# Kernel tuning notes

Measured on AMD Instinct MI355X. Metric: run time of the kernel, lower is better.

## Reference

```python
import jax, jax.numpy as jnp
import numpy as np

B, C, H, W = 1, 256, 48, 64
HW = H * W
HIDDEN, CTX = 128, 64
LEVELS, RADIUS = 4, 4
WIN = 2 * RADIUS + 1
P = WIN * WIN                     # 81 lookup points per level
CORR_DIM = P * LEVELS             # 324
TOP_K = 3
ITERS = 4
STEP_ROT, STEP_TRANS = 0.02, 0.02


def _sample_templates():
    # 12 directions x 3 scales + identity = 37 pose perturbations (as in __init__)
    base = [([0,0,0],[1,0,0]),([0,0,0],[-1,0,0]),([0,0,0],[0,1,0]),([0,0,0],[0,-1,0]),
            ([0,0,0],[0,0,1]),([0,0,0],[0,0,-1]),([1,0,0],[0,0,0]),([-1,0,0],[0,0,0]),
            ([0,1,0],[0,0,0]),([0,-1,0],[0,0,0]),([0,0,1],[0,0,0]),([0,0,-1],[0,0,0])]
    scales = np.array([0.25, 1.0, 4.0], np.float32)
    rot = np.repeat(np.array([r for r, _ in base], np.float32), 3, axis=0)
    trs = np.repeat(np.array([t for _, t in base], np.float32), 3, axis=0)
    sc = np.tile(scales, 12)
    axes = rot / np.clip(np.linalg.norm(rot, axis=1, keepdims=True), 1e-8, None)
    ha = STEP_ROT * sc / 2.0
    dq = np.stack([np.cos(ha), axes[:, 0]*np.sin(ha), axes[:, 1]*np.sin(ha), axes[:, 2]*np.sin(ha)], -1)
    dt = trs * (STEP_TRANS * sc[:, None])
    dq = np.concatenate([dq, [[1., 0., 0., 0.]]], 0)
    dt = np.concatenate([dt, [[0., 0., 0.]]], 0)
    return jnp.asarray(dq), jnp.asarray(dt)

DQ, DT = _sample_templates()     # (37,4), (37,3)
N_SAMPLES = DQ.shape[0]


def qmul(q, r):
    w1, x1, y1, z1 = jnp.moveaxis(q, -1, 0)
    w2, x2, y2, z2 = jnp.moveaxis(r, -1, 0)
    return jnp.stack([w1*w2 - x1*x2 - y1*y2 - z1*z2,
                      w1*x2 + x1*w2 + y1*z2 - z1*y2,
                      w1*y2 - x1*z2 + y1*w2 + z1*x2,
                      w1*z2 + x1*y2 - y1*x2 + z1*w2], -1)


def qapply(q, v):
    qv = jnp.concatenate([jnp.zeros(v.shape[:-1] + (1,), v.dtype), v], -1)
    qc = q * jnp.array([1., -1., -1., -1.], q.dtype)
    return qmul(qmul(q, qv), qc)[..., 1:]


def quat_to_R(q):
    w, x, y, z = jnp.moveaxis(q, -1, 0)
    R = jnp.stack([1-2*(y*y+z*z), 2*(x*y-w*z), 2*(x*z+w*y),
                   2*(x*y+w*z), 1-2*(x*x+z*z), 2*(y*z-w*x),
                   2*(x*z-w*y), 2*(y*z+w*x), 1-2*(x*x+y*y)], -1)
    return R.reshape(q.shape[:-1] + (3, 3))


def conv3(x, w, b):
    y = jax.lax.conv_general_dilated(x, w, (1, 1), 'SAME',
                                     dimension_numbers=('NCHW', 'OIHW', 'NCHW'))
    return y + b[None, :, None, None]


def bilinear_lookup(corr_flat, Hl, Wl, x, y):
    # corr_flat: (B,HW,Hl*Wl); x,y: (B,N,HW,P) -> (B,N,HW,P), zero padding outside
    x0 = jnp.floor(x)
    y0 = jnp.floor(y)
    out = jnp.zeros(x.shape, corr_flat.dtype)
    def gather(idx):
        g = lambda ix: jnp.take_along_axis(corr_flat, ix, axis=-1)
        return jax.vmap(g, in_axes=1, out_axes=1)(idx)   # vmap over N, no corr copy
    for dx_, dy_ in ((0, 0), (1, 0), (0, 1), (1, 1)):
        xi = x0 + dx_
        yi = y0 + dy_
        wgt = (1 - jnp.abs(x - xi)) * (1 - jnp.abs(y - yi))
        valid = (xi >= 0) & (xi < Wl) & (yi >= 0) & (yi < Hl)
        idx = (jnp.clip(yi, 0, Hl - 1) * Wl + jnp.clip(xi, 0, Wl - 1)).astype(jnp.int32)
        out = out + jnp.where(valid, wgt, 0.0) * gather(idx)
    return out


def _forward(fmap_rgb, fmap_depth, depth, context, intrinsics,
             Wz, bz, Wr, br, Wq, bq, Wh, bh, Wfc, bfc):
    f32 = jnp.float32
    fx = 60. + 40. * intrinsics[:, 0]
    fy = 60. + 40. * intrinsics[:, 1]
    cx = W / 2. + 4. * (intrinsics[:, 2] - 0.5)
    cy = H / 2. + 4. * (intrinsics[:, 3] - 0.5)
    d = 4.0 + 20.0 * depth                                  # (B,H,W) metric depth

    # 4D correlation pyramid: corr[b,i,:,:] = <fmap_depth pixel i, fmap_rgb>
    fd = fmap_depth.reshape(B, C, HW).transpose(0, 2, 1)    # (B,HW,C)
    corr = jnp.einsum('bic,bchw->bihw', fd, fmap_rgb) / jnp.sqrt(f32(C))
    pyramid = []
    cl, Hl, Wl = corr, H, W
    for _ in range(LEVELS):
        pyramid.append((cl.reshape(B, HW, Hl * Wl), Hl, Wl))
        cl = cl.reshape(B, HW, Hl // 2, 2, Wl // 2, 2).mean(axis=(3, 5))
        Hl //= 2
        Wl //= 2

    # back-projected depth points (B,HW,3)
    vv, uu = jnp.meshgrid(jnp.arange(H, dtype=f32), jnp.arange(W, dtype=f32), indexing='ij')
    uu = uu.reshape(HW)
    vv = vv.reshape(HW)
    df = d.reshape(B, HW)
    X = jnp.stack([(uu[None] - cx[:, None]) / fx[:, None] * df,
                   (vv[None] - cy[:, None]) / fy[:, None] * df, df], -1)

    off = jnp.arange(-RADIUS, RADIUS + 1, dtype=f32)
    oy, ox = jnp.meshgrid(off, off, indexing='ij')
    ox = ox.reshape(P)
    oy = oy.reshape(P)

    pose = jnp.tile(jnp.array([1., 0., 0., 0., 0., 0., 0.], f32)[None, :], (B, 1))
    h = jnp.zeros((B, HIDDEN, H, W), f32)

    for _ in range(ITERS):
        qc, tc = pose[:, :4], pose[:, 4:7]
        quats = qmul(qc[:, None, :], DQ[None])              # (B,N,4)
        quats = quats / jnp.linalg.norm(quats, axis=-1, keepdims=True)
        trans = tc[:, None, :] + qapply(qc[:, None, :], DT[None])
        Rm = quat_to_R(quats)                               # (B,N,3,3)
        Xc = jnp.einsum('bnij,bpj->bnpi', Rm, X) + trans[:, :, None, :]
        z = jnp.clip(Xc[..., 2], 0.1, None)
        u = fx[:, None, None] * Xc[..., 0] / z + cx[:, None, None]   # (B,N,HW)
        v = fy[:, None, None] * Xc[..., 1] / z + cy[:, None, None]
        feats = []
        for lvl, (cfl, Hl_, Wl_) in enumerate(pyramid):
            s = f32(2 ** lvl)
            xl = u[..., None] / s + ox
            yl = v[..., None] / s + oy
            feats.append(bilinear_lookup(cfl, Hl_, Wl_, xl, yl))
        cf = jnp.concatenate(feats, -1)                     # (B,N,HW,CORR_DIM)
        conf = cf.mean(axis=(2, 3))                         # (B,N) sample confidence
        topv, topi = jax.lax.top_k(conf, TOP_K)
        wk = jax.nn.softmax(topv, axis=-1)                  # confidence-weighted top-K
        idx = jnp.broadcast_to(topi[:, :, None, None], (B, TOP_K, HW, CORR_DIM))
        sel = jnp.take_along_axis(cf, idx, axis=1)
        fused = (wk[:, :, None, None] * sel).sum(1)         # (B,HW,CORR_DIM)
        fused = fused.transpose(0, 2, 1).reshape(B, CORR_DIM, H, W)

        # ConvGRU update
        x_in = jnp.concatenate([fused, context], 1)
        hx = jnp.concatenate([h, x_in], 1)
        zg = jax.nn.sigmoid(conv3(hx, Wz, bz))
        rg = jax.nn.sigmoid(conv3(hx, Wr, br))
        qg = jnp.tanh(conv3(jnp.concatenate([rg * h, x_in], 1), Wq, bq))
        h = (1 - zg) * h + zg * qg

        # 7D pose delta head + quaternion/Lie-style update
        feat = jax.nn.relu(conv3(h, Wh, bh)).mean(axis=(2, 3))
        delta = 0.01 * (feat @ Wfc + bfc)                   # (B,7)
        dq = jnp.concatenate([1.0 + delta[:, :1], delta[:, 1:4]], -1)
        dq = dq / jnp.linalg.norm(dq, axis=-1, keepdims=True)
        tn = tc + qapply(qc, delta[:, 4:7])
        qn = qmul(qc, dq)
        qn = qn / jnp.linalg.norm(qn, axis=-1, keepdims=True)
        pose = jnp.concatenate([qn, tn], -1)
    return pose


def setup_inputs() -> dict:
    key = jax.random.key(0)
    ks = jax.random.split(key, 12)
    rn = lambda k, shape, s=1.0: s * jax.random.normal(k, shape, jnp.float32)
    Gin = HIDDEN + CORR_DIM + CTX
    sc = 1.0 / np.sqrt(Gin * 9)
    sh = 1.0 / np.sqrt(HIDDEN * 9)
    return {
        'fmap_rgb': rn(ks[0], (B, C, H, W)),
        'fmap_depth': rn(ks[1], (B, C, H, W)),
        'depth': jax.random.uniform(ks[2], (B, H, W), jnp.float32),
        'context': rn(ks[3], (B, CTX, H, W)),
        'intrinsics': jax.random.uniform(ks[4], (B, 4), jnp.float32),
        'Wz': rn(ks[5], (HIDDEN, Gin, 3, 3), sc), 'bz': jnp.zeros((HIDDEN,), jnp.float32),
        'Wr': rn(ks[6], (HIDDEN, Gin, 3, 3), sc), 'br': jnp.zeros((HIDDEN,), jnp.float32),
        'Wq': rn(ks[7], (HIDDEN, Gin, 3, 3), sc), 'bq': jnp.zeros((HIDDEN,), jnp.float32),
        'Wh': rn(ks[8], (HIDDEN, HIDDEN, 3, 3), sh), 'bh': jnp.zeros((HIDDEN,), jnp.float32),
        'Wfc': rn(ks[9], (HIDDEN, 7), 1.0 / np.sqrt(HIDDEN)), 'bfc': jnp.zeros((7,), jnp.float32),
    }


def reference(fmap_rgb, fmap_depth, depth, context, intrinsics,
              Wz, bz, Wr, br, Wq, bq, Wh, bh, Wfc, bfc):
    return _forward(fmap_rgb, fmap_depth, depth, context, intrinsics,
                    Wz, bz, Wr, br, Wq, bq, Wh, bh, Wfc, bfc)
```

## Files before the change

### kernel.cpp

```cpp
#include <hip/hip_runtime.h>
#include <math.h>

constexpr int kH = 48, kW = 64, kHW = 3072, kC = 256;
constexpr int kHidden = 128, kCtx = 64;
constexpr int kP = 81, kCorrDim = 324;
constexpr int kNS = 37, kIters = 4;
constexpr int kGin = kHidden + kCorrDim + kCtx;
constexpr int kWp2 = 66, kHp2 = 50, kPix = 3300;
constexpr int kCF = 416;
constexpr int kCHh = 128;

constexpr int kSB0 = 0, kSB1 = 4292, kSB2 = 5720, kSB3 = 6292, kSBTot = 6580;
constexpr int kHB0 = 0, kHB1 = 3552, kHB2 = 4560, kHB3 = 4872, kHBTot = 4980;

constexpr size_t U_CORR0 = 0;
constexpr size_t U_CORR1 = U_CORR0 + (size_t)kHW * 3072;
constexpr size_t U_CORR2 = U_CORR1 + (size_t)kHW * 768;
constexpr size_t U_CORR3 = U_CORR2 + (size_t)kHW * 192;
constexpr size_t U_END0  = U_CORR3 + (size_t)kHW * 48;
constexpr size_t F_X     = U_END0 / 2;
constexpr size_t F_H     = F_X + (size_t)kHW * 3;
constexpr size_t F_ZPRE  = F_H + (size_t)kHidden * kHW;
constexpr size_t F_END1  = F_ZPRE + (size_t)kHidden * kHW;
constexpr size_t U_FCT   = F_END1 * 2;
constexpr size_t U_HT    = U_FCT + (size_t)kPix * kCF;
constexpr size_t U_RHT   = U_HT + (size_t)kPix * kCHh;
constexpr size_t U_PZR   = U_RHT + (size_t)kPix * kCHh;
constexpr size_t U_PQ    = U_PZR + (size_t)16 * 9 * 17 * 512;
constexpr size_t U_PH    = U_PQ + (size_t)8 * 9 * 17 * 512;
constexpr size_t U_END2  = U_PH + (size_t)8 * 9 * 4 * 512;
constexpr size_t F_BZR   = U_END2 / 2 + 1;
constexpr size_t F_CONF  = F_BZR + 256;
constexpr size_t F_POSE  = F_CONF + 64;
constexpr size_t F_FEAT  = F_POSE + 16;
constexpr size_t F_END3  = F_FEAT + 128;
constexpr size_t U_FDT   = F_END3 * 2;
constexpr size_t U_QT    = U_FDT + (size_t)kHW * kC;
constexpr size_t U_SBOX  = U_FDT;

typedef __attribute__((ext_vector_type(8))) short short8;
typedef __attribute__((ext_vector_type(4))) float f32x4;

__device__ inline unsigned short f2b(float f) {
  unsigned int u = __float_as_uint(f);
  unsigned int r = u + 0x7FFF + ((u >> 16) & 1);
  return (unsigned short)(r >> 16);
}
__device__ inline float b2f(unsigned short u) {
  return __uint_as_float(((unsigned int)u) << 16);
}
__device__ inline int clampi(int v, int lo, int hi) { return min(max(v, lo), hi); }

__constant__ float c_rot[12][3] = {
  {0,0,0},{0,0,0},{0,0,0},{0,0,0},{0,0,0},{0,0,0},
  {1,0,0},{-1,0,0},{0,1,0},{0,-1,0},{0,0,1},{0,0,-1}};
__constant__ float c_trs[12][3] = {
  {1,0,0},{-1,0,0},{0,1,0},{0,-1,0},{0,0,1},{0,0,-1},
  {0,0,0},{0,0,0},{0,0,0},{0,0,0},{0,0,0},{0,0,0}};

__device__ inline void d_qmul(const float* q, const float* r, float* o) {
  o[0] = q[0]*r[0] - q[1]*r[1] - q[2]*r[2] - q[3]*r[3];
  o[1] = q[0]*r[1] + q[1]*r[0] + q[2]*r[3] - q[3]*r[2];
  o[2] = q[0]*r[2] - q[1]*r[3] + q[2]*r[0] + q[3]*r[1];
  o[3] = q[0]*r[3] + q[1]*r[2] - q[2]*r[1] + q[3]*r[0];
}
__device__ inline void d_qapply(const float* q, const float* v, float* o) {
  float a0 = -q[1]*v[0] - q[2]*v[1] - q[3]*v[2];
  float a1 =  q[0]*v[0] + q[2]*v[2] - q[3]*v[1];
  float a2 =  q[0]*v[1] - q[1]*v[2] + q[3]*v[0];
  float a3 =  q[0]*v[2] + q[1]*v[1] - q[2]*v[0];
  o[0] = -a0*q[1] + a1*q[0] - a2*q[3] + a3*q[2];
  o[1] = -a0*q[2] + a1*q[3] + a2*q[0] - a3*q[1];
  o[2] = -a0*q[3] - a1*q[2] + a2*q[1] + a3*q[0];
}
__device__ inline void d_intr(const float* intr, float& fx, float& fy, float& cx, float& cy) {
  fx = 60.f + 40.f*intr[0];
  fy = 60.f + 40.f*intr[1];
  cx = 32.f + 4.f*(intr[2] - 0.5f);
  cy = 24.f + 4.f*(intr[3] - 0.5f);
}
__device__ inline void sample_Rt(int t, const float* __restrict__ pose, float* S) {
  float qc[4] = {pose[0], pose[1], pose[2], pose[3]};
  float tc[3] = {pose[4], pose[5], pose[6]};
  float dq[4], dt[3];
  if (t == 36) {
    dq[0] = 1.f; dq[1] = dq[2] = dq[3] = 0.f;
    dt[0] = dt[1] = dt[2] = 0.f;
  } else {
    int j = t / 3, k = t % 3;
    float sc = (k == 0) ? 0.25f : ((k == 1) ? 1.f : 4.f);
    float rx = c_rot[j][0], ry = c_rot[j][1], rz = c_rot[j][2];
    float nrm = sqrtf(rx*rx + ry*ry + rz*rz);
    float axn = fmaxf(nrm, 1e-8f);
    float ax = rx / axn, ay = ry / axn, az = rz / axn;
    float ha = 0.02f * sc * 0.5f;
    float sh = sinf(ha), ch = cosf(ha);
    dq[0] = ch; dq[1] = ax * sh; dq[2] = ay * sh; dq[3] = az * sh;
    dt[0] = c_trs[j][0] * (0.02f * sc);
    dt[1] = c_trs[j][1] * (0.02f * sc);
    dt[2] = c_trs[j][2] * (0.02f * sc);
  }
  float qn[4];
  d_qmul(qc, dq, qn);
  float inv = 1.f / sqrtf(qn[0]*qn[0] + qn[1]*qn[1] + qn[2]*qn[2] + qn[3]*qn[3]);
  qn[0] *= inv; qn[1] *= inv; qn[2] *= inv; qn[3] *= inv;
  float tr[3];
  d_qapply(qc, dt, tr);
  float w = qn[0], x = qn[1], y = qn[2], z = qn[3];
  S[0] = 1.f - 2.f*(y*y + z*z); S[1] = 2.f*(x*y - w*z);       S[2] = 2.f*(x*z + w*y);
  S[3] = 2.f*(x*y + w*z);       S[4] = 1.f - 2.f*(x*x + z*z); S[5] = 2.f*(y*z - w*x);
  S[6] = 2.f*(x*z - w*y);       S[7] = 2.f*(y*z + w*x);       S[8] = 1.f - 2.f*(x*x + y*y);
  S[9]  = tc[0] + tr[0];
  S[10] = tc[1] + tr[1];
  S[11] = tc[2] + tr[2];
}
__device__ inline void project_uv(const float* S, const float* Xp, const float* intr,
                                  float& u, float& v) {
  float xc0 = S[0]*Xp[0] + S[1]*Xp[1] + S[2]*Xp[2] + S[9];
  float xc1 = S[3]*Xp[0] + S[4]*Xp[1] + S[5]*Xp[2] + S[10];
  float xc2 = S[6]*Xp[0] + S[7]*Xp[1] + S[8]*Xp[2] + S[11];
  float z = fmaxf(xc2, 0.1f);
  float fx, fy, cx, cy;
  d_intr(intr, fx, fy, cx, cy);
  u = fx * xc0 / z + cx;
  v = fy * xc1 / z + cy;
}

__global__ void init_k(const float* __restrict__ ctx, const float* __restrict__ bz,
                       const float* __restrict__ br, const float* __restrict__ depth,
                       const float* __restrict__ intr, float* __restrict__ h,
                       unsigned int* __restrict__ zbase, unsigned short* __restrict__ fcT,
                       float* __restrict__ bzr, float* __restrict__ X,
                       float* __restrict__ conf, float* __restrict__ feat,
                       float* __restrict__ pose) {
  const size_t nz = ((size_t)kPix * (kCF + 2 * kCHh)) / 2;
  for (size_t i = blockIdx.x * blockDim.x + threadIdx.x; i < nz;
       i += (size_t)gridDim.x * blockDim.x)
    zbase[i] = 0;
  int idx = blockIdx.x * blockDim.x + threadIdx.x;
  if (idx < kHidden * kHW) h[idx] = 0.f;
  if (idx < kHW) {
    float fx, fy, cx, cy;
    d_intr(intr, fx, fy, cx, cy);
    float d = 4.f + 20.f * depth[idx];
    float u = (float)(idx % kW), v = (float)(idx / kW);
    X[idx*3+0] = (u - cx) / fx * d;
    X[idx*3+1] = (v - cy) / fy * d;
    X[idx*3+2] = d;
  }
  if (idx < 256) bzr[idx] = (idx < 128) ? bz[idx] : br[idx - 128];
  if (idx < 64) conf[idx] = 0.f;
  if (idx < 128) feat[idx] = 0.f;
  if (idx == 0) {
    pose[0] = 1.f;
    for (int j = 1; j < 7; ++j) pose[j] = 0.f;
  }
}
__global__ void initctx_k(const float* __restrict__ ctx, unsigned short* __restrict__ fcT) {
  int idx = blockIdx.x * blockDim.x + threadIdx.x;
  if (idx < kHW * 64) {
    int p = idx >> 6, c = idx & 63;
    int ppix = ((p >> 6) + 1) * kWp2 + (p & 63) + 1;
    fcT[(size_t)ppix * kCF + kCorrDim + c] = f2b(ctx[(size_t)c * kHW + p]);
  }
}

__global__ void pack_k(const float* __restrict__ W0, const float* __restrict__ W1,
                       int ocSplit, int OC, int NCH, int Cin,
                       unsigned short* __restrict__ P) {
  int idx = blockIdx.x * blockDim.x + threadIdx.x;
  int total = (OC / 16) * 9 * NCH * 64;
  if (idx >= total) return;
  int g = idx & 3;
  int m = (idx >> 2) & 15;
  int rest = idx >> 6;
  int cc = rest % NCH;
  int rest2 = rest / NCH;
  int tap = rest2 % 9;
  int ot = rest2 / 9;
  int oc = ot * 16 + m;
  union { unsigned short u[8]; uint4 q; } v;
#pragma unroll
  for (int j = 0; j < 8; ++j) {
    int ci = cc * 32 + g * 8 + j;
    float w = 0.f;
    if (ci < Cin)
      w = (oc < ocSplit) ? W0[((size_t)oc * Cin + ci) * 9 + tap]
                         : W1[((size_t)(oc - ocSplit) * Cin + ci) * 9 + tap];
    v.u[j] = f2b(w);
  }
  *(uint4*)&P[(size_t)idx * 8] = v.q;
}

__global__ __launch_bounds__(256) void t_bf16_k(const float* __restrict__ src,
                                                unsigned short* __restrict__ dst) {
  __shared__ float t[64][65];
  const int tid = threadIdx.x;
  const int p0 = blockIdx.x * 64, c0 = blockIdx.y * 64;
  const int tx = tid & 63, ty = tid >> 6;
  for (int cl = ty; cl < 64; cl += 4)
    t[cl][tx] = src[(size_t)(c0 + cl) * kHW + p0 + tx];
  __syncthreads();
  for (int pl = ty; pl < 64; pl += 4)
    dst[(size_t)(p0 + pl) * kC + c0 + tx] = f2b(t[tx][pl]);
}

__global__ __launch_bounds__(256) void corr_mfma_k(const unsigned short* __restrict__ fdT,
                                                   const unsigned short* __restrict__ qT,
                                                   unsigned short* __restrict__ Cg) {
  const int tid = threadIdx.x;
  const int wv = tid >> 6, lane = tid & 63;
  const int m = lane & 15, kg = lane >> 4;
  const int i0 = blockIdx.y * 128 + wv * 32;
  const int q0 = blockIdx.x * 128;

  f32x4 acc[2][8];
#pragma unroll
  for (int t = 0; t < 2; ++t)
#pragma unroll
    for (int u = 0; u < 8; ++u) acc[t][u] = (f32x4){0.f, 0.f, 0.f, 0.f};

#pragma unroll
  for (int kc = 0; kc < 8; ++kc) {
    const int kb = kc * 32 + kg * 8;
    short8 a[2], b[8];
#pragma unroll
    for (int t = 0; t < 2; ++t)
      a[t] = *(const short8*)&fdT[(size_t)(i0 + t * 16 + m) * kC + kb];
#pragma unroll
    for (int u = 0; u < 8; ++u)
      b[u] = *(const short8*)&qT[(size_t)(q0 + u * 16 + m) * kC + kb];
#pragma unroll
    for (int t = 0; t < 2; ++t)
#pragma unroll
      for (int u = 0; u < 8; ++u)
        acc[t][u] = __builtin_amdgcn_mfma_f32_16x16x32_bf16(a[t], b[u], acc[t][u], 0, 0, 0);
  }
  const float S = 0.0625f;
#pragma unroll
  for (int t = 0; t < 2; ++t)
#pragma unroll
    for (int u = 0; u < 8; ++u)
#pragma unroll
      for (int r = 0; r < 4; ++r)
        Cg[(size_t)(i0 + t * 16 + kg * 4 + r) * kHW + q0 + u * 16 + m] = f2b(acc[t][u][r] * S);
}

template<int HL>
__device__ inline void colpref(float* base, int Wp) {
  float v[HL];
#pragma unroll
  for (int y = 0; y < HL; ++y) v[y] = base[(size_t)y * Wp];
  float run = 0.f;
#pragma unroll
  for (int y = 0; y < HL; ++y) {
    run += v[y];
    base[(size_t)y * Wp] = run;
  }
}

__global__ __launch_bounds__(256) void boxbuild_k(const unsigned short* __restrict__ corr0,
                                                  unsigned short* __restrict__ corr1,
                                                  unsigned short* __restrict__ corr2,
                                                  unsigned short* __restrict__ corr3,
                                                  unsigned short* __restrict__ Sbox) {
  __shared__ float pyr[4080];
  __shared__ float hb[kHBTot];
  const int i = blockIdx.x;
  const int tid = threadIdx.x;
  const int wv = tid >> 6, lane = tid & 63;

  for (int idx = tid; idx < 3072; idx += 256)
    pyr[idx] = b2f(corr0[(size_t)i * 3072 + idx]);
  __syncthreads();

  for (int c = tid; c < 768; c += 256) {
    int y = c >> 5, x = c & 31;
    float v = 0.25f * (pyr[(2*y)*64 + 2*x] + pyr[(2*y)*64 + 2*x + 1] +
                       pyr[(2*y+1)*64 + 2*x] + pyr[(2*y+1)*64 + 2*x + 1]);
    unsigned short b = f2b(v);
    corr1[(size_t)i * 768 + c] = b;
    pyr[3072 + c] = b2f(b);
  }
  __syncthreads();
  for (int c = tid; c < 192; c += 256) {
    int y = c >> 4, x = c & 15;
    const float* p = pyr + 3072;
    float v = 0.25f * (p[(2*y)*32 + 2*x] + p[(2*y)*32 + 2*x + 1] +
                       p[(2*y+1)*32 + 2*x] + p[(2*y+1)*32 + 2*x + 1]);
    unsigned short b = f2b(v);
    corr2[(size_t)i * 192 + c] = b;
    pyr[3840 + c] = b2f(b);
  }
  __syncthreads();
  for (int c = tid; c < 48; c += 256) {
    int y = c >> 3, x = c & 7;
    const float* p = pyr + 3840;
    float v = 0.25f * (p[(2*y)*16 + 2*x] + p[(2*y)*16 + 2*x + 1] +
                       p[(2*y+1)*16 + 2*x] + p[(2*y+1)*16 + 2*x + 1]);
    unsigned short b = f2b(v);
    corr3[(size_t)i * 48 + c] = b;
    pyr[4032 + c] = b2f(b);
  }
  __syncthreads();

  const int lvl_off[4] = {0, 3072, 3840, 4032};
  for (int r = wv; r < 90; r += 4) {
    int lvl, y;
    if (r < 48)      { lvl = 0; y = r; }
    else if (r < 72) { lvl = 1; y = r - 48; }
    else if (r < 84) { lvl = 2; y = r - 72; }
    else             { lvl = 3; y = r - 84; }
    const int Wl = kW >> lvl;
    float* row = &pyr[lvl_off[lvl] + y * Wl];
    float v = (lane < Wl) ? row[lane] : 0.f;
#pragma unroll
    for (int o = 1; o < 64; o <<= 1) {
      float tv = __shfl_up(v, o, 64);
      if (lane >= o) v += tv;
    }
    if (lane < Wl) row[lane] = v;
  }
  __syncthreads();

  for (int c = tid; c < 3552; c += 256) {
    int y = c / 74, as = c % 74;
    const float* pref = &pyr[y * 64];
    float Hv = 0.f;
    if (as >= 1) Hv = pref[min(63, as - 1)];
    if (as >= 10) Hv -= pref[as - 10];
    hb[kHB0 + c] = Hv;
  }
  for (int c = tid; c < 1008; c += 256) {
    int y = c / 42, as = c % 42;
    const float* pref = &pyr[3072 + y * 32];
    float Hv = 0.f;
    if (as >= 1) Hv = pref[min(31, as - 1)];
    if (as >= 10) Hv -= pref[as - 10];
    hb[kHB1 + c] = Hv;
  }
  for (int c = tid; c < 312; c += 256) {
    int y = c / 26, as = c % 26;
    const float* pref = &pyr[3840 + y * 16];
    float Hv = 0.f;
    if (as >= 1) Hv = pref[min(15, as - 1)];
    if (as >= 10) Hv -= pref[as - 10];
    hb[kHB2 + c] = Hv;
  }
  for (int c = tid; c < 108; c += 256) {
    int y = c / 18, as = c % 18;
    const float* pref = &pyr[4032 + y * 8];
    float Hv = 0.f;
    if (as >= 1) Hv = pref[min(7, as - 1)];
    if (as >= 10) Hv -= pref[as - 10];
    hb[kHB3 + c] = Hv;
  }
  __syncthreads();

  if (tid < 160) {
    if (tid < 74)       colpref<48>(hb + kHB0 + tid, 74);
    else if (tid < 116) colpref<24>(hb + kHB1 + (tid - 74), 42);
    else if (tid < 142) colpref<12>(hb + kHB2 + (tid - 116), 26);
    else                colpref<6>(hb + kHB3 + (tid - 142), 18);
  }
  __syncthreads();

  unsigned short* out = Sbox + (size_t)i * kSBTot;
  for (int c = tid; c < 4292; c += 256) {
    int bp = c / 74, as = c % 74;
    const float* col = &hb[kHB0 + as];
    float S = 0.f;
    if (bp >= 1) S = col[min(47, bp - 1) * 74];
    if (bp >= 10) S -= col[(bp - 10) * 74];
    out[kSB0 + c] = f2b(S);
  }
  for (int c = tid; c < 1428; c += 256) {
    int bp = c / 42, as = c % 42;
    const float* col = &hb[kHB1 + as];
    float S = 0.f;
    if (bp >= 1) S = col[min(23, bp - 1) * 42];
    if (bp >= 10) S -= col[(bp - 10) * 42];
    out[kSB1 + c] = f2b(S);
  }
  for (int c = tid; c < 572; c += 256) {
    int bp = c / 26, as = c % 26;
    const float* col = &hb[kHB2 + as];
    float S = 0.f;
    if (bp >= 1) S = col[min(11, bp - 1) * 26];
    if (bp >= 10) S -= col[(bp - 10) * 26];
    out[kSB2 + c] = f2b(S);
  }
  for (int c = tid; c < 288; c += 256) {
    int bp = c / 18, as = c % 18;
    const float* col = &hb[kHB3 + as];
    float S = 0.f;
    if (bp >= 1) S = col[min(5, bp - 1) * 18];
    if (bp >= 10) S -= col[(bp - 10) * 18];
    out[kSB3 + c] = f2b(S);
  }
}

__global__ __launch_bounds__(256) void conf_k(const unsigned short* __restrict__ Sbox,
                                              const float* __restrict__ X,
                                              const float* __restrict__ pose,
                                              const float* __restrict__ intr,
                                              float* __restrict__ conf) {
  const int idx = blockIdx.x * 256 + threadIdx.x;
  const int n = idx / kHW, i = idx - n * kHW;
  float S[12];
  sample_Rt(n, pose, S);
  float Xp[3] = {X[i*3], X[i*3+1], X[i*3+2]};
  float u, v;
  project_uv(S, Xp, intr, u, v);
  const unsigned short* sb = Sbox + (size_t)i * kSBTot;
  float tot = 0.f;
#pragma unroll
  for (int l = 0; l < 4; ++l) {
    const int Wp = (kW >> l) + 10, Hp = (kH >> l) + 10;
    const int so = (l == 0) ? kSB0 : (l == 1) ? kSB1 : (l == 2) ? kSB2 : kSB3;
    const float s = (float)(1 << l);
    const float bx = u / s, by = v / s;
    const float fbx = floorf(bx), fby = floorf(by);
    const int x0 = (int)fbx, y0 = (int)fby;
    const float fx = bx - fbx, fy = by - fby;
    const int xa = clampi(x0 + 5, 0, Wp - 1), xb = clampi(x0 + 6, 0, Wp - 1);
    const int ya = clampi(y0 + 5, 0, Hp - 1), yb = clampi(y0 + 6, 0, Hp - 1);
    const float s00 = b2f(sb[so + ya * Wp + xa]), s10 = b2f(sb[so + ya * Wp + xb]);
    const float s01 = b2f(sb[so + yb * Wp + xa]), s11 = b2f(sb[so + yb * Wp + xb]);
    tot += (1.f - fx) * (1.f - fy) * s00 + fx * (1.f - fy) * s10 +
           (1.f - fx) * fy * s01 + fx * fy * s11;
  }
#pragma unroll
  for (int o = 32; o; o >>= 1) tot += __shfl_xor(tot, o, 64);
  if ((threadIdx.x & 63) == 0) atomicAdd(&conf[n], tot);
}

__global__ __launch_bounds__(256) void fused_k(const unsigned short* __restrict__ corr0,
                                               const unsigned short* __restrict__ corr1,
                                               const unsigned short* __restrict__ corr2,
                                               const unsigned short* __restrict__ corr3,
                                               const float* __restrict__ X,
                                               const float* __restrict__ pose,
                                               const float* __restrict__ intr,
                                               const float* __restrict__ conf,
                                               unsigned short* __restrict__ fcT) {
  __shared__ float win[12][10][12];
  __shared__ float s_fx[12], s_fy[12];
  __shared__ int   s_ix[12], s_iy[12];
  __shared__ float s_w[3];
  __shared__ int   s_id[3];
  const int i = blockIdx.x;
  const int tid = threadIdx.x;

  if (tid == 0) {
    const float scale = 1.f / ((float)kHW * (float)kCorrDim);
    float c[kNS];
    for (int n = 0; n < kNS; ++n) c[n] = conf[n] * scale;
    int id[3] = {-1, -1, -1};
    float v[3];
    for (int k = 0; k < 3; ++k) {
      float best = -1e30f;
      int bi = -1;
      for (int n = 0; n < kNS; ++n) {
        if (n == id[0] || n == id[1] || n == id[2]) continue;
        if (c[n] > best) { best = c[n]; bi = n; }
      }
      v[k] = best;
      id[k] = bi;
    }
    float m = v[0];
    float e0 = expf(v[0] - m), e1 = expf(v[1] - m), e2 = expf(v[2] - m);
    float s = e0 + e1 + e2;
    s_w[0] = e0 / s; s_w[1] = e1 / s; s_w[2] = e2 / s;
    s_id[0] = id[0]; s_id[1] = id[1]; s_id[2] = id[2];
  }
  __syncthreads();

  if (tid < 3) {
    int n = s_id[tid];
    float S[12];
    sample_Rt(n, pose, S);
    float Xp[3] = {X[i*3], X[i*3+1], X[i*3+2]};
    float u, v;
    project_uv(S, Xp, intr, u, v);
#pragma unroll
    for (int l = 0; l < 4; ++l) {
      float s = (float)(1 << l);
      float bx = u / s, by = v / s;
      float fbx = floorf(bx), fby = floorf(by);
      s_ix[tid*4 + l] = (int)fbx;
      s_iy[tid*4 + l] = (int)fby;
      s_fx[tid*4 + l] = bx - fbx;
      s_fy[tid*4 + l] = by - fby;
    }
  }
  __syncthreads();

  for (int sidx = tid; sidx < 1200; sidx += 256) {
    const int w = sidx / 100, rem = sidx % 100;
    const int rr = rem / 10, cc = rem % 10;
    const int lvl = w & 3;
    const int Wl = kW >> lvl, Hl = kH >> lvl;
    const unsigned short* base =
        (lvl == 0) ? corr0 : (lvl == 1) ? corr1 : (lvl == 2) ? corr2 : corr3;
    const int y = s_iy[w] - 4 + rr;
    const int x = s_ix[w] - 4 + cc;
    float v = 0.f;
    if (y >= 0 && y < Hl && x >= 0 && x < Wl)
      v = b2f(base[(size_t)i * (Hl * Wl) + y * Wl + x]);
    win[w][rr][cc] = v;
  }
  __syncthreads();

  const int ppix = ((i >> 6) + 1) * kWp2 + (i & 63) + 1;
  for (int d = tid; d < kCorrDim; d += 256) {
    const int lvl = d / kP;
    const int o = d % kP;
    const int oyi = o / 9, oxi = o % 9;
    float val = 0.f;
#pragma unroll
    for (int k = 0; k < 3; ++k) {
      const int w = k * 4 + lvl;
      const float fx = s_fx[w], fy = s_fy[w];
      const float w00 = (1.f - fx) * (1.f - fy), w10 = fx * (1.f - fy);
      const float w01 = (1.f - fx) * fy, w11 = fx * fy;
      val += s_w[k] * (w00 * win[w][oyi][oxi] + w10 * win[w][oyi][oxi + 1] +
                       w01 * win[w][oyi + 1][oxi] + w11 * win[w][oyi + 1][oxi + 1]);
    }
    fcT[(size_t)ppix * kCF + d] = f2b(val);
  }
}

template<int NCHH, int NCHF>
__device__ inline void conv_core16(const unsigned short* __restrict__ srcH,
                                   const unsigned short* __restrict__ srcF,
                                   const unsigned short* __restrict__ A,
                                   int y, int xbase, int ot, int lane,
                                   f32x4& acc) {
  const int m = lane & 15, kg = lane >> 4;
  constexpr int NCH = NCHH + NCHF;
  const unsigned short* a_base = A + (size_t)ot * (9 * NCH * 512) + m * 32 + kg * 8;
  const int pix0 = (y + 1) * kWp2 + (xbase + 1) + m;
#pragma unroll
  for (int tap = 0; tap < 9; ++tap) {
    const int dy = tap / 3 - 1, dx = tap % 3 - 1;
    const int po = pix0 + dy * kWp2 + dx;
    const unsigned short* bh0 = srcH + (size_t)po * kCHh + kg * 8;
    const unsigned short* bf0 = srcF + (size_t)po * kCF + kg * 8;
#pragma unroll
    for (int cc = 0; cc < NCH; ++cc) {
      const int s = tap * NCH + cc;
      short8 a = *(const short8*)(a_base + (size_t)s * 512);
      short8 b = (cc < NCHH) ? *(const short8*)(bh0 + cc * 32)
                             : *(const short8*)(bf0 + (cc - NCHH) * 32);
      acc = __builtin_amdgcn_mfma_f32_16x16x32_bf16(a, b, acc, 0, 0, 0);
    }
  }
}

__global__ __launch_bounds__(256) void conv_zr_k(const unsigned short* __restrict__ hT,
                                                 const unsigned short* __restrict__ fcT,
                                                 const unsigned short* __restrict__ P,
                                                 const float* __restrict__ bzr,
                                                 float* __restrict__ zpre,
                                                 const float* __restrict__ hbuf,
                                                 unsigned short* __restrict__ rhT) {
  const int tid = threadIdx.x;
  const int wv = tid >> 6, lane = tid & 63;
  const int y = blockIdx.y >> 2, xbase = (blockIdx.y & 3) * 16;
  const int ot = blockIdx.x * 4 + wv;
  f32x4 acc = {0.f, 0.f, 0.f, 0.f};
  conv_core16<4, 13>(hT, fcT, P, y, xbase, ot, lane, acc);
  const int m = lane & 15, kg = lane >> 4;
#pragma unroll
  for (int r = 0; r < 4; ++r) {
    const int oc = ot * 16 + kg * 4 + r;
    const int pxx = xbase + m;
    const int px = y * kW + pxx;
    const float val = acc[r] + bzr[oc];
    if (oc < kHidden) {
      zpre[(size_t)oc * kHW + px] = val;
    } else {
      const float rg = 1.f / (1.f + expf(-val));
      const int ppix = (y + 1) * kWp2 + pxx + 1;
      rhT[(size_t)ppix * kCHh + oc - kHidden] =
          f2b(rg * hbuf[(size_t)(oc - kHidden) * kHW + px]);
    }
  }
}

__global__ __launch_bounds__(256) void conv_q_k(const unsigned short* __restrict__ rhT,
                                                const unsigned short* __restrict__ fcT,
                                                unsigned short* __restrict__ hT,
                                                const unsigned short* __restrict__ P,
                                                const float* __restrict__ bq,
                                                const float* __restrict__ zpre,
                                                float* __restrict__ hbuf) {
  const int tid = threadIdx.x;
  const int wv = tid >> 6, lane = tid & 63;
  const int y = blockIdx.y >> 2, xbase = (blockIdx.y & 3) * 16;
  const int ot = blockIdx.x * 4 + wv;
  f32x4 acc = {0.f, 0.f, 0.f, 0.f};
  conv_core16<4, 13>(rhT, fcT, P, y, xbase, ot, lane, acc);
  const int m = lane & 15, kg = lane >> 4;
#pragma unroll
  for (int r = 0; r < 4; ++r) {
    const int oc = ot * 16 + kg * 4 + r;
    const int pxx = xbase + m;
    const int px = y * kW + pxx;
    const size_t off = (size_t)oc * kHW + px;
    const float q = acc[r] + bq[oc];
    const float zg = 1.f / (1.f + expf(-zpre[off]));
    const float hn = (1.f - zg) * hbuf[off] + zg * tanhf(q);
    hbuf[off] = hn;
    const int ppix = (y + 1) * kWp2 + pxx + 1;
    hT[(size_t)ppix * kCHh + oc] = f2b(hn);
  }
}

__global__ __launch_bounds__(256) void conv_h_k(const unsigned short* __restrict__ hT,
                                                const unsigned short* __restrict__ P,
                                                const float* __restrict__ bh,
                                                float* __restrict__ feat) {
  const int tid = threadIdx.x;
  const int wv = tid >> 6, lane = tid & 63;
  const int y = blockIdx.y >> 2, xbase = (blockIdx.y & 3) * 16;
  const int ot = blockIdx.x * 4 + wv;
  f32x4 acc = {0.f, 0.f, 0.f, 0.f};
  conv_core16<4, 0>(hT, hT, P, y, xbase, ot, lane, acc);
  const int m = lane & 15, kg = lane >> 4;
#pragma unroll
  for (int r = 0; r < 4; ++r) {
    const int oc = ot * 16 + kg * 4 + r;
    float v = fmaxf(acc[r] + bh[oc], 0.f);
    v += __shfl_xor(v, 1, 64);
    v += __shfl_xor(v, 2, 64);
    v += __shfl_xor(v, 4, 64);
    v += __shfl_xor(v, 8, 64);
    if (m == 0) atomicAdd(&feat[oc], v);
  }
}

__global__ void pose_update_k(float* __restrict__ feat, float* __restrict__ conf,
                              const float* __restrict__ Wfc,
                              const float* __restrict__ bfc, float* __restrict__ pose,
                              float* __restrict__ out) {
  __shared__ float s_d[7];
  int t = threadIdx.x;
  if (t < 7) {
    float s = 0.f;
    const float inv = 1.f / (float)kHW;
    for (int k = 0; k < kHidden; ++k) s += (feat[k] * inv) * Wfc[k * 7 + t];
    s_d[t] = 0.01f * (s + bfc[t]);
  }
  __syncthreads();
  if (t < kHidden) feat[t] = 0.f;
  if (t < 64) conf[t] = 0.f;
  if (t != 0) return;
  float qc[4] = {pose[0], pose[1], pose[2], pose[3]};
  float tc[3] = {pose[4], pose[5], pose[6]};
  float dq[4] = {1.f + s_d[0], s_d[1], s_d[2], s_d[3]};
  float inv = 1.f / sqrtf(dq[0]*dq[0] + dq[1]*dq[1] + dq[2]*dq[2] + dq[3]*dq[3]);
  dq[0] *= inv; dq[1] *= inv; dq[2] *= inv; dq[3] *= inv;
  float dv[3] = {s_d[4], s_d[5], s_d[6]};
  float rv[3];
  d_qapply(qc, dv, rv);
  float tn[3] = {tc[0] + rv[0], tc[1] + rv[1], tc[2] + rv[2]};
  float qn[4];
  d_qmul(qc, dq, qn);
  float inv2 = 1.f / sqrtf(qn[0]*qn[0] + qn[1]*qn[1] + qn[2]*qn[2] + qn[3]*qn[3]);
  qn[0] *= inv2; qn[1] *= inv2; qn[2] *= inv2; qn[3] *= inv2;
  pose[0] = qn[0]; pose[1] = qn[1]; pose[2] = qn[2]; pose[3] = qn[3];
  pose[4] = tn[0]; pose[5] = tn[1]; pose[6] = tn[2];
  out[0] = qn[0]; out[1] = qn[1]; out[2] = qn[2]; out[3] = qn[3];
  out[4] = tn[0]; out[5] = tn[1]; out[6] = tn[2];
}

extern "C" void kernel_launch(void* const* d_in, const int* in_sizes, int n_in,
                              void* d_out, int out_size, void* d_ws, size_t ws_size,
                              hipStream_t stream) {
  const float* frgb  = (const float*)d_in[0];
  const float* fdep  = (const float*)d_in[1];
  const float* depth = (const float*)d_in[2];
  const float* ctx   = (const float*)d_in[3];
  const float* intr  = (const float*)d_in[4];
  const float* Wz = (const float*)d_in[5];
  const float* bz = (const float*)d_in[6];
  const float* Wr = (const float*)d_in[7];
  const float* br = (const float*)d_in[8];
  const float* Wq = (const float*)d_in[9];
  const float* bq = (const float*)d_in[10];
  const float* Wh = (const float*)d_in[11];
  const float* bh = (const float*)d_in[12];
  const float* Wfc = (const float*)d_in[13];
  const float* bfc = (const float*)d_in[14];
  float* outp = (float*)d_out;

  float* ws = (float*)d_ws;
  unsigned short* us = (unsigned short*)d_ws;
  unsigned short* corr0 = us + U_CORR0;
  unsigned short* corr1 = us + U_CORR1;
  unsigned short* corr2 = us + U_CORR2;
  unsigned short* corr3 = us + U_CORR3;
  float* X    = ws + F_X;
  float* hbuf = ws + F_H;
  float* zpre = ws + F_ZPRE;
  unsigned short* fcT = us + U_FCT;
  unsigned short* hT  = us + U_HT;
  unsigned short* rhT = us + U_RHT;
  unsigned short* Pzr = us + U_PZR;
  unsigned short* Pq  = us + U_PQ;
  unsigned short* Ph  = us + U_PH;
  float* bzr  = ws + F_BZR;
  float* conf = ws + F_CONF;
  float* pose = ws + F_POSE;
  float* feat = ws + F_FEAT;
  unsigned short* fdT  = us + U_FDT;
  unsigned short* qT   = us + U_QT;
  unsigned short* Sbox = us + U_SBOX;

  init_k<<<1536, 256, 0, stream>>>(ctx, bz, br, depth, intr, hbuf,
                                   (unsigned int*)fcT, fcT, bzr, X, conf, feat, pose);
  initctx_k<<<768, 256, 0, stream>>>(ctx, fcT);
  pack_k<<<(16 * 9 * 17 * 64 + 255) / 256, 256, 0, stream>>>(Wz, Wr, 128, 256, 17,
                                                             kGin, Pzr);
  pack_k<<<(8 * 9 * 17 * 64 + 255) / 256, 256, 0, stream>>>(Wq, Wq, 128, 128, 17,
                                                            kGin, Pq);
  pack_k<<<(8 * 9 * 4 * 64 + 255) / 256, 256, 0, stream>>>(Wh, Wh, 128, 128, 4,
                                                           kHidden, Ph);
  t_bf16_k<<<dim3(48, 4), 256, 0, stream>>>(fdep, fdT);
  t_bf16_k<<<dim3(48, 4), 256, 0, stream>>>(frgb, qT);
  corr_mfma_k<<<dim3(24, 24), 256, 0, stream>>>(fdT, qT, corr0);
  boxbuild_k<<<kHW, 256, 0, stream>>>(corr0, corr1, corr2, corr3, Sbox);

  for (int it = 0; it < kIters; ++it) {
    conf_k<<<444, 256, 0, stream>>>(Sbox, X, pose, intr, conf);
    fused_k<<<kHW, 256, 0, stream>>>(corr0, corr1, corr2, corr3, X, pose, intr,
                                     conf, fcT);
    conv_zr_k<<<dim3(4, 192), 256, 0, stream>>>(hT, fcT, Pzr, bzr, zpre, hbuf, rhT);
    conv_q_k<<<dim3(2, 192), 256, 0, stream>>>(rhT, fcT, hT, Pq, bq, zpre, hbuf);
    conv_h_k<<<dim3(2, 192), 256, 0, stream>>>(hT, Ph, bh, feat);
    pose_update_k<<<1, 128, 0, stream>>>(feat, conf, Wfc, bfc, pose, outp);
  }
}
```

Measured before the change: 917.4 us.

## Widen conv tiles to 32 pixels and split K across wave pairs

The GRU conv kernels now have each wave compute two 16-pixel MFMA tiles that share one weight fragment, so each weight load is reused across 32 pixels. In the z/r and q convs, the input-channel chunks are split between two waves, and the partial sums are combined through shared memory after a block barrier. The grid is reshaped so the block count stays similar. This halves weight traffic per output, at the cost of more registers, an LDS reduction step, and half the waves idling during the epilogue.

```diff
diff --git a/kernel.cpp b/kernel.cpp
--- a/kernel.cpp
+++ b/kernel.cpp
@@ -531,15 +531,14 @@
   }
 }
 
-template<int NCHH, int NCHF>
-__device__ inline void conv_core16(const unsigned short* __restrict__ srcH,
+template<int CCB, int CCE, int NCHH, int NCHTOT>
+__device__ inline void conv_core32(const unsigned short* __restrict__ srcH,
                                    const unsigned short* __restrict__ srcF,
                                    const unsigned short* __restrict__ A,
                                    int y, int xbase, int ot, int lane,
-                                   f32x4& acc) {
+                                   f32x4 (&acc)[2]) {
   const int m = lane & 15, kg = lane >> 4;
-  constexpr int NCH = NCHH + NCHF;
-  const unsigned short* a_base = A + (size_t)ot * (9 * NCH * 512) + m * 32 + kg * 8;
+  const unsigned short* a_base = A + (size_t)ot * (9 * NCHTOT * 512) + m * 32 + kg * 8;
   const int pix0 = (y + 1) * kWp2 + (xbase + 1) + m;
 #pragma unroll
   for (int tap = 0; tap < 9; ++tap) {
@@ -548,12 +547,19 @@
     const unsigned short* bh0 = srcH + (size_t)po * kCHh + kg * 8;
     const unsigned short* bf0 = srcF + (size_t)po * kCF + kg * 8;
 #pragma unroll
-    for (int cc = 0; cc < NCH; ++cc) {
-      const int s = tap * NCH + cc;
+    for (int cc = CCB; cc < CCE; ++cc) {
+      const int s = tap * NCHTOT + cc;
       short8 a = *(const short8*)(a_base + (size_t)s * 512);
-      short8 b = (cc < NCHH) ? *(const short8*)(bh0 + cc * 32)
-                             : *(const short8*)(bf0 + (cc - NCHH) * 32);
-      acc = __builtin_amdgcn_mfma_f32_16x16x32_bf16(a, b, acc, 0, 0, 0);
+      short8 b0, b1;
+      if (cc < NCHH) {
+        b0 = *(const short8*)(bh0 + cc * 32);
+        b1 = *(const short8*)(bh0 + 16 * kCHh + cc * 32);
+      } else {
+        b0 = *(const short8*)(bf0 + (cc - NCHH) * 32);
+        b1 = *(const short8*)(bf0 + 16 * kCF + (cc - NCHH) * 32);
+      }
+      acc[0] = __builtin_amdgcn_mfma_f32_16x16x32_bf16(a, b0, acc[0], 0, 0, 0);
+      acc[1] = __builtin_amdgcn_mfma_f32_16x16x32_bf16(a, b1, acc[1], 0, 0, 0);
     }
   }
 }
@@ -565,28 +571,41 @@
                                                  float* __restrict__ zpre,
                                                  const float* __restrict__ hbuf,
                                                  unsigned short* __restrict__ rhT) {
+  __shared__ f32x4 red[2][2][64];
   const int tid = threadIdx.x;
   const int wv = tid >> 6, lane = tid & 63;
-  const int y = blockIdx.y >> 2, xbase = (blockIdx.y & 3) * 16;
-  const int ot = blockIdx.x * 4 + wv;
-  f32x4 acc = {0.f, 0.f, 0.f, 0.f};
-  conv_core16<4, 13>(hT, fcT, P, y, xbase, ot, lane, acc);
+  const int p = wv >> 1, half = wv & 1;
+  const int y = blockIdx.y >> 1, xbase = (blockIdx.y & 1) * 32;
+  const int ot = blockIdx.x * 2 + p;
+  f32x4 acc[2] = {{0.f,0.f,0.f,0.f},{0.f,0.f,0.f,0.f}};
+  if (half == 0) conv_core32<0, 9, 4, 17>(hT, fcT, P, y, xbase, ot, lane, acc);
+  else           conv_core32<9, 17, 4, 17>(hT, fcT, P, y, xbase, ot, lane, acc);
+  if (half == 1) {
+    red[p][0][lane] = acc[0];
+    red[p][1][lane] = acc[1];
+  }
+  __syncthreads();
+  if (half != 0) return;
+  acc[0] += red[p][0][lane];
+  acc[1] += red[p][1][lane];
   const int m = lane & 15, kg = lane >> 4;
 #pragma unroll
-  for (int r = 0; r < 4; ++r) {
-    const int oc = ot * 16 + kg * 4 + r;
-    const int pxx = xbase + m;
-    const int px = y * kW + pxx;
-    const float val = acc[r] + bzr[oc];
-    if (oc < kHidden) {
-      zpre[(size_t)oc * kHW + px] = val;
-    } else {
-      const float rg = 1.f / (1.f + expf(-val));
-      const int ppix = (y + 1) * kWp2 + pxx + 1;
-      rhT[(size_t)ppix * kCHh + oc - kHidden] =
-          f2b(rg * hbuf[(size_t)(oc - kHidden) * kHW + px]);
+  for (int t = 0; t < 2; ++t)
+#pragma unroll
+    for (int r = 0; r < 4; ++r) {
+      const int oc = ot * 16 + kg * 4 + r;
+      const int pxx = xbase + t * 16 + m;
+      const int px = y * kW + pxx;
+      const float val = acc[t][r] + bzr[oc];
+      if (oc < kHidden) {
+        zpre[(size_t)oc * kHW + px] = val;
+      } else {
+        const float rg = 1.f / (1.f + expf(-val));
+        const int ppix = (y + 1) * kWp2 + pxx + 1;
+        rhT[(size_t)ppix * kCHh + oc - kHidden] =
+            f2b(rg * hbuf[(size_t)(oc - kHidden) * kHW + px]);
+      }
     }
-  }
 }
 
 __global__ __launch_bounds__(256) void conv_q_k(const unsigned short* __restrict__ rhT,
@@ -596,26 +615,39 @@
                                                 const float* __restrict__ bq,
                                                 const float* __restrict__ zpre,
                                                 float* __restrict__ hbuf) {
+  __shared__ f32x4 red[2][2][64];
   const int tid = threadIdx.x;
   const int wv = tid >> 6, lane = tid & 63;
-  const int y = blockIdx.y >> 2, xbase = (blockIdx.y & 3) * 16;
-  const int ot = blockIdx.x * 4 + wv;
-  f32x4 acc = {0.f, 0.f, 0.f, 0.f};
-  conv_core16<4, 13>(rhT, fcT, P, y, xbase, ot, lane, acc);
+  const int p = wv >> 1, half = wv & 1;
+  const int y = blockIdx.y >> 1, xbase = (blockIdx.y & 1) * 32;
+  const int ot = blockIdx.x * 2 + p;
+  f32x4 acc[2] = {{0.f,0.f,0.f,0.f},{0.f,0.f,0.f,0.f}};
+  if (half == 0) conv_core32<0, 9, 4, 17>(rhT, fcT, P, y, xbase, ot, lane, acc);
+  else           conv_core32<9, 17, 4, 17>(rhT, fcT, P, y, xbase, ot, lane, acc);
+  if (half == 1) {
+    red[p][0][lane] = acc[0];
+    red[p][1][lane] = acc[1];
+  }
+  __syncthreads();
+  if (half != 0) return;
+  acc[0] += red[p][0][lane];
+  acc[1] += red[p][1][lane];
   const int m = lane & 15, kg = lane >> 4;
 #pragma unroll
-  for (int r = 0; r < 4; ++r) {
-    const int oc = ot * 16 + kg * 4 + r;
-    const int pxx = xbase + m;
-    const int px = y * kW + pxx;
-    const size_t off = (size_t)oc * kHW + px;
-    const float q = acc[r] + bq[oc];
-    const float zg = 1.f / (1.f + expf(-zpre[off]));
-    const float hn = (1.f - zg) * hbuf[off] + zg * tanhf(q);
-    hbuf[off] = hn;
-    const int ppix = (y + 1) * kWp2 + pxx + 1;
-    hT[(size_t)ppix * kCHh + oc] = f2b(hn);
-  }
+  for (int t = 0; t < 2; ++t)
+#pragma unroll
+    for (int r = 0; r < 4; ++r) {
+      const int oc = ot * 16 + kg * 4 + r;
+      const int pxx = xbase + t * 16 + m;
+      const int px = y * kW + pxx;
+      const size_t off = (size_t)oc * kHW + px;
+      const float q = acc[t][r] + bq[oc];
+      const float zg = 1.f / (1.f + expf(-zpre[off]));
+      const float hn = (1.f - zg) * hbuf[off] + zg * tanhf(q);
+      hbuf[off] = hn;
+      const int ppix = (y + 1) * kWp2 + pxx + 1;
+      hT[(size_t)ppix * kCHh + oc] = f2b(hn);
+    }
 }
 
 __global__ __launch_bounds__(256) void conv_h_k(const unsigned short* __restrict__ hT,
@@ -624,15 +656,16 @@
                                                 float* __restrict__ feat) {
   const int tid = threadIdx.x;
   const int wv = tid >> 6, lane = tid & 63;
-  const int y = blockIdx.y >> 2, xbase = (blockIdx.y & 3) * 16;
+  const int y = blockIdx.y >> 1, xbase = (blockIdx.y & 1) * 32;
   const int ot = blockIdx.x * 4 + wv;
-  f32x4 acc = {0.f, 0.f, 0.f, 0.f};
-  conv_core16<4, 0>(hT, hT, P, y, xbase, ot, lane, acc);
+  f32x4 acc[2] = {{0.f,0.f,0.f,0.f},{0.f,0.f,0.f,0.f}};
+  conv_core32<0, 4, 4, 4>(hT, hT, P, y, xbase, ot, lane, acc);
   const int m = lane & 15, kg = lane >> 4;
 #pragma unroll
   for (int r = 0; r < 4; ++r) {
     const int oc = ot * 16 + kg * 4 + r;
-    float v = fmaxf(acc[r] + bh[oc], 0.f);
+    const float bv = bh[oc];
+    float v = fmaxf(acc[0][r] + bv, 0.f) + fmaxf(acc[1][r] + bv, 0.f);
     v += __shfl_xor(v, 1, 64);
     v += __shfl_xor(v, 2, 64);
     v += __shfl_xor(v, 4, 64);
@@ -737,9 +770,9 @@
     conf_k<<<444, 256, 0, stream>>>(Sbox, X, pose, intr, conf);
     fused_k<<<kHW, 256, 0, stream>>>(corr0, corr1, corr2, corr3, X, pose, intr,
                                      conf, fcT);
-    conv_zr_k<<<dim3(4, 192), 256, 0, stream>>>(hT, fcT, Pzr, bzr, zpre, hbuf, rhT);
-    conv_q_k<<<dim3(2, 192), 256, 0, stream>>>(rhT, fcT, hT, Pq, bq, zpre, hbuf);
-    conv_h_k<<<dim3(2, 192), 256, 0, stream>>>(hT, Ph, bh, feat);
+    conv_zr_k<<<dim3(8, 96), 256, 0, stream>>>(hT, fcT, Pzr, bzr, zpre, hbuf, rhT);
+    conv_q_k<<<dim3(4, 96), 256, 0, stream>>>(rhT, fcT, hT, Pq, bq, zpre, hbuf);
+    conv_h_k<<<dim3(2, 96), 256, 0, stream>>>(hT, Ph, bh, feat);
     pose_update_k<<<1, 128, 0, stream>>>(feat, conf, Wfc, bfc, pose, outp);
   }
 }
```

New measurement: 821.9 us. 1.12x faster.
